# Optimization experiments

Measured on AMD Instinct MI355X. Metric: run time of the kernel, lower is better.

Reference implementation:

```python
import math
import jax, jax.numpy as jnp
import numpy as np

B, S_IN, S_OUT, D_IN, D_OUT = 8, 4096, 1024, 128, 128
EPS = 1e-5


def setup_inputs() -> dict:
    key = jax.random.key(0)
    k0, k1, k2, k3 = jax.random.split(key, 4)
    x = jax.random.normal(k0, (B, S_IN, D_IN), dtype=jnp.float32)
    M = jax.random.uniform(k1, (D_OUT, D_IN), minval=-0.5, maxval=0.5, dtype=jnp.float32)
    P = jax.random.uniform(k2, (D_OUT, D_OUT), minval=-0.1, maxval=0.1, dtype=jnp.float32)
    Linker = jax.random.uniform(k3, (S_IN, S_OUT), minval=-0.1, maxval=0.1, dtype=jnp.float32)
    gamma = jnp.ones((D_OUT,), dtype=jnp.float32)   # LayerNorm weight
    beta = jnp.zeros((D_OUT,), dtype=jnp.float32)   # LayerNorm bias
    return {"x": x, "M": M, "P": P, "Linker": Linker, "gamma": gamma, "beta": beta}


def reference(x, M, P, Linker, gamma, beta):
    # x: (B, S, in_dim) -> out: (B, S_out, out_dim)
    Bsz, S, _ = x.shape
    D = M.shape[0]
    x_trans = x @ M.T                                   # (B, S, D)
    mu = jnp.mean(x_trans, axis=-1, keepdims=True)
    var = jnp.var(x_trans, axis=-1, keepdims=True)      # biased, matches torch LayerNorm
    x_trans = (x_trans - mu) / jnp.sqrt(var + EPS) * gamma + beta
    # periods[i, j] = i*D + j + 2 (registered buffer)
    idx = jnp.arange(D)
    periods = (idx[:, None] * D + idx[None, :] + 2).astype(jnp.float32)  # (D, D)
    k = jnp.arange(S, dtype=jnp.float32)[:, None, None]                   # (S, 1, 1)
    phi = jnp.cos(2.0 * math.pi * k / periods)                            # (S, D, D)
    M_k = P[None, :, :] * phi                                             # (S, D, D)
    Nk = jnp.einsum('bsj,sij->bsi', x_trans, M_k)                         # (B, S, D)
    out = jnp.einsum('bsi,st->bti', Nk, Linker)                           # (B, S_out, D)
    return out
```

## Files before the change

### kernel.cpp

```cpp
#include <hip/hip_runtime.h>
#include <math.h>

#define B_SZ   8
#define S_INN  4096
#define S_OUTT 1024
#define DD     128
#define EPS_LN 1e-5f

typedef _Float16 h2 __attribute__((ext_vector_type(2)));
typedef _Float16 h4 __attribute__((ext_vector_type(4)));
typedef _Float16 h8 __attribute__((ext_vector_type(8)));
typedef float f32x4 __attribute__((ext_vector_type(4)));

#define XN_OFF   0
#define NK16_OFF 4194304
#define NT_OFF   6291456
#define LT_OFF   8388608

__device__ __forceinline__ void gload16(const void* g, void* l) {
    __builtin_amdgcn_global_load_lds(
        (const __attribute__((address_space(1))) unsigned int*)g,
        (__attribute__((address_space(3))) unsigned int*)l, 16, 0, 0);
}

__device__ __forceinline__ float fdot2_(h2 a, h2 b, float c) {
#if __has_builtin(__builtin_amdgcn_fdot2)
    return __builtin_amdgcn_fdot2(a, b, c, false);
#else
    return fmaf((float)a[0], (float)b[0], fmaf((float)a[1], (float)b[1], c));
#endif
}

__global__ __launch_bounds__(256) void kA(const float* __restrict__ x,
                                          const float* __restrict__ M,
                                          const float* __restrict__ gamma,
                                          const float* __restrict__ beta,
                                          _Float16* __restrict__ xn16) {
    __shared__ float Ms[128 * 128];

    const int tid = threadIdx.x;
    #pragma unroll
    for (int k = 0; k < 16; ++k) {
        int e4 = tid + k * 256;
        int i  = e4 >> 5;
        int j4 = e4 & 31;
        float4 v = *(const float4*)&M[i * DD + j4 * 4];
        int igp = (i >> 4) & 7;
        int qp  = (i >> 2) & 3;
        int cp  = i & 3;
        int col = (qp * 8 + igp) * 4 + cp;
        Ms[(j4 * 4 + 0) * 128 + col] = v.x;
        Ms[(j4 * 4 + 1) * 128 + col] = v.y;
        Ms[(j4 * 4 + 2) * 128 + col] = v.z;
        Ms[(j4 * 4 + 3) * 128 + col] = v.w;
    }
    __syncthreads();

    const int ig = tid & 7;
    const int rg = tid >> 3;
    const int row0 = blockIdx.x * 64 + rg * 2;

    float acc[2][16];
    #pragma unroll
    for (int rr = 0; rr < 2; ++rr)
        #pragma unroll
        for (int k = 0; k < 16; ++k) acc[rr][k] = 0.f;

    const float4* xr[2];
    #pragma unroll
    for (int rr = 0; rr < 2; ++rr) xr[rr] = (const float4*)&x[(size_t)(row0 + rr) * DD];

    for (int j4 = 0; j4 < 32; ++j4) {
        float xvf[2][4];
        #pragma unroll
        for (int rr = 0; rr < 2; ++rr) {
            float4 t = xr[rr][j4];
            xvf[rr][0] = t.x; xvf[rr][1] = t.y; xvf[rr][2] = t.z; xvf[rr][3] = t.w;
        }
        #pragma unroll
        for (int c = 0; c < 4; ++c) {
            const float* Mrow = &Ms[(j4 * 4 + c) * 128];
            #pragma unroll
            for (int q = 0; q < 4; ++q) {
                const float4 mv = *(const float4*)&Mrow[(q * 8 + ig) * 4];
                #pragma unroll
                for (int rr = 0; rr < 2; ++rr) {
                    acc[rr][q * 4 + 0] = fmaf(xvf[rr][c], mv.x, acc[rr][q * 4 + 0]);
                    acc[rr][q * 4 + 1] = fmaf(xvf[rr][c], mv.y, acc[rr][q * 4 + 1]);
                    acc[rr][q * 4 + 2] = fmaf(xvf[rr][c], mv.z, acc[rr][q * 4 + 2]);
                    acc[rr][q * 4 + 3] = fmaf(xvf[rr][c], mv.w, acc[rr][q * 4 + 3]);
                }
            }
        }
    }

    float g[16], be[16];
    #pragma unroll
    for (int q = 0; q < 4; ++q) {
        float4 gv = *(const float4*)&gamma[ig * 16 + q * 4];
        float4 bv = *(const float4*)&beta[ig * 16 + q * 4];
        g[q*4+0]=gv.x; g[q*4+1]=gv.y; g[q*4+2]=gv.z; g[q*4+3]=gv.w;
        be[q*4+0]=bv.x; be[q*4+1]=bv.y; be[q*4+2]=bv.z; be[q*4+3]=bv.w;
    }
    #pragma unroll
    for (int rr = 0; rr < 2; ++rr) {
        float s1 = 0.f, s2 = 0.f;
        #pragma unroll
        for (int k = 0; k < 16; ++k) { s1 += acc[rr][k]; s2 = fmaf(acc[rr][k], acc[rr][k], s2); }
        #pragma unroll
        for (int m = 1; m < 8; m <<= 1) {
            s1 += __shfl_xor(s1, m, 64);
            s2 += __shfl_xor(s2, m, 64);
        }
        float mu  = s1 * (1.f / 128.f);
        float var = s2 * (1.f / 128.f) - mu * mu;
        float rstd = rsqrtf(var + EPS_LN);
        _Float16* dst = &xn16[(size_t)(row0 + rr) * DD + ig * 16];
        #pragma unroll
        for (int q = 0; q < 4; ++q) {
            h4 hv;
            hv[0] = (_Float16)((acc[rr][q*4+0] - mu) * rstd * g[q*4+0] + be[q*4+0]);
            hv[1] = (_Float16)((acc[rr][q*4+1] - mu) * rstd * g[q*4+1] + be[q*4+1]);
            hv[2] = (_Float16)((acc[rr][q*4+2] - mu) * rstd * g[q*4+2] + be[q*4+2]);
            hv[3] = (_Float16)((acc[rr][q*4+3] - mu) * rstd * g[q*4+3] + be[q*4+3]);
            *(h4*)&dst[q * 4] = hv;
        }
    }
}

__global__ __launch_bounds__(256, 4) void kB(const _Float16* __restrict__ xn16,
                                             const float* __restrict__ P,
                                             _Float16* __restrict__ nk16) {
    const int s = blockIdx.x;
    __shared__ _Float16 Ps[128 * 136];
    __shared__ _Float16 xs[64 * 16];

    const int tid = threadIdx.x;
    {
        int j  = tid & 127;
        int bh = (tid >> 7) * 4;
        int j2 = j >> 1;
        int slot = (j2 & 15) * 4 + (j2 >> 4);
        #pragma unroll
        for (int bo = 0; bo < 4; ++bo) {
            int b = bh + bo;
            xs[slot * 16 + b * 2 + (j & 1)] = xn16[((size_t)b * S_INN + s) * DD + j];
        }
    }
    #pragma unroll
    for (int k = 0; k < 16; ++k) {
        int e4 = tid + k * 256;
        int ip = e4 >> 5, j4 = e4 & 31;
        float4 v = *(const float4*)&P[ip * DD + j4 * 4];
        h4 hv = { (_Float16)v.x, (_Float16)v.y, (_Float16)v.z, (_Float16)v.w };
        *(h4*)&Ps[ip * 136 + j4 * 4] = hv;
    }
    __syncthreads();

    const int il = tid >> 2;
    const int jq = tid & 3;
    const float kf = (float)s;
    const float pb0 = (float)(il * DD + jq * 32 + 2);

    float acc0[8] = {0.f,0.f,0.f,0.f,0.f,0.f,0.f,0.f};
    float acc1[8] = {0.f,0.f,0.f,0.f,0.f,0.f,0.f,0.f};

    #pragma unroll
    for (int j8 = 0; j8 < 4; ++j8) {
        const int j0 = jq * 32 + j8 * 8;
        h8 p0 = *(const h8*)&Ps[il * 136 + j0];
        h8 p1 = *(const h8*)&Ps[(il + 64) * 136 + j0];

        h2 w0[4], w1[4];
        #pragma unroll
        for (int cp = 0; cp < 4; ++cp) {
            float wv0[2], wv1[2];
            #pragma unroll
            for (int u = 0; u < 2; ++u) {
                int c = cp * 2 + u;
                float pf0 = pb0 + (float)(j8 * 8 + c);
                float iv0 = __builtin_amdgcn_rcpf(pf0);
                float q0  = floorf(kf * iv0);
                float rm0 = fmaf(-q0, pf0, kf);
                wv0[u] = (float)p0[c] * __builtin_amdgcn_cosf(rm0 * iv0);
                float pf1 = pf0 + 8192.f;
                float iv1 = __builtin_amdgcn_rcpf(pf1);
                float q1  = floorf(kf * iv1);
                float rm1 = fmaf(-q1, pf1, kf);
                wv1[u] = (float)p1[c] * __builtin_amdgcn_cosf(rm1 * iv1);
            }
            w0[cp] = h2{ (_Float16)wv0[0], (_Float16)wv0[1] };
            w1[cp] = h2{ (_Float16)wv1[0], (_Float16)wv1[1] };
        }

        #pragma unroll
        for (int jp = 0; jp < 4; ++jp) {
            int slot = (j8 * 4 + jp) * 4 + jq;
            const h8 xlo = *(const h8*)&xs[slot * 16];
            const h8 xhi = *(const h8*)&xs[slot * 16 + 8];
            #pragma unroll
            for (int b = 0; b < 4; ++b) {
                h2 xa = h2{ xlo[b * 2], xlo[b * 2 + 1] };
                h2 xb = h2{ xhi[b * 2], xhi[b * 2 + 1] };
                acc0[b]     = fdot2_(w0[jp], xa, acc0[b]);
                acc0[b + 4] = fdot2_(w0[jp], xb, acc0[b + 4]);
                acc1[b]     = fdot2_(w1[jp], xa, acc1[b]);
                acc1[b + 4] = fdot2_(w1[jp], xb, acc1[b + 4]);
            }
        }
    }

    #pragma unroll
    for (int m = 1; m < 4; m <<= 1) {
        #pragma unroll
        for (int b = 0; b < 8; ++b) {
            acc0[b] += __shfl_xor(acc0[b], m, 64);
            acc1[b] += __shfl_xor(acc1[b], m, 64);
        }
    }
    if (jq == 0) {
        #pragma unroll
        for (int b = 0; b < 8; ++b) {
            nk16[((size_t)b * S_INN + s) * DD + il]      = (_Float16)acc0[b];
            nk16[((size_t)b * S_INN + s) * DD + il + 64] = (_Float16)acc1[b];
        }
    }
}

__global__ __launch_bounds__(256) void kXf(const float* __restrict__ src,
                                           _Float16* __restrict__ dst,
                                           int R, int C) {
    const size_t sb = (size_t)blockIdx.z * (size_t)R * C;
    const int r0 = blockIdx.x * 64, c0 = blockIdx.y * 64;
    __shared__ float tile[64][67];
    const int tid = threadIdx.x;
    {
        const int lr = tid >> 2, lc = (tid & 3) * 16;
        const float4* srow = (const float4*)&src[sb + (size_t)(r0 + lr) * C + c0 + lc];
        float4 v0 = srow[0], v1 = srow[1], v2 = srow[2], v3 = srow[3];
        *(float4*)&tile[lr][lc +  0] = v0;
        *(float4*)&tile[lr][lc +  4] = v1;
        *(float4*)&tile[lr][lc +  8] = v2;
        *(float4*)&tile[lr][lc + 12] = v3;
    }
    __syncthreads();
    {
        const int wc = tid >> 2, wsx = (tid & 3) * 16;
        h8 o0, o1;
        #pragma unroll
        for (int k = 0; k < 8; ++k) o0[k] = (_Float16)tile[wsx + k][wc];
        #pragma unroll
        for (int k = 0; k < 8; ++k) o1[k] = (_Float16)tile[wsx + 8 + k][wc];
        _Float16* drow = &dst[sb + (size_t)(c0 + wc) * R + r0 + wsx];
        *(h8*)&drow[0] = o0;
        *(h8*)&drow[8] = o1;
    }
}

__global__ __launch_bounds__(256) void kXh(const _Float16* __restrict__ src,
                                           _Float16* __restrict__ dst,
                                           int R, int C) {
    const size_t sb = (size_t)blockIdx.z * (size_t)R * C;
    const int r0 = blockIdx.x * 64, c0 = blockIdx.y * 64;
    __shared__ _Float16 tile[64][74];
    const int tid = threadIdx.x;
    {
        const int lr = tid >> 2, lc = (tid & 3) * 16;
        const h8* srow = (const h8*)&src[sb + (size_t)(r0 + lr) * C + c0 + lc];
        h8 v0 = srow[0], v1 = srow[1];
        *(h8*)&tile[lr][lc + 0] = v0;
        *(h8*)&tile[lr][lc + 8] = v1;
    }
    __syncthreads();
    {
        const int wc = tid >> 2, wsx = (tid & 3) * 16;
        h8 o0, o1;
        #pragma unroll
        for (int k = 0; k < 8; ++k) o0[k] = tile[wsx + k][wc];
        #pragma unroll
        for (int k = 0; k < 8; ++k) o1[k] = tile[wsx + 8 + k][wc];
        _Float16* drow = &dst[sb + (size_t)(c0 + wc) * R + r0 + wsx];
        *(h8*)&drow[0] = o0;
        *(h8*)&drow[8] = o1;
    }
}

__global__ __launch_bounds__(512) void kC(const _Float16* __restrict__ NT,
                                          const _Float16* __restrict__ LT,
                                          float* __restrict__ part) {
    __shared__ _Float16 lds_pool[4 * 8192];

    const int tid  = threadIdx.x;
    const int lane = tid & 63;
    const int w    = tid >> 6;
    const int wm   = w >> 2;
    const int wn   = w & 3;
    const int lr   = lane & 15;
    const int lh   = lane >> 4;

    const int mt = blockIdx.x >> 3;
    const int nt = blockIdx.x & 7;
    const int kz = blockIdx.y;
    const int t0 = mt * 128;
    const int n0 = nt * 128;
    const int sbase = kz * 1024;

    const int swz = (lr & 7) << 4;

    f32x4 acc[4][2];
    #pragma unroll
    for (int m = 0; m < 4; ++m)
        #pragma unroll
        for (int n = 0; n < 2; ++n) acc[m][n] = (f32x4){0.f, 0.f, 0.f, 0.f};

    auto stage = [&](int buf, int s0) {
        _Float16* base = &lds_pool[buf * 16384];
        #pragma unroll
        for (int ro = 0; ro < 2; ++ro) {
            int idx = tid + ro * 512;
            int r   = idx >> 3;
            int kb  = idx & 7;
            int skb = kb ^ (r & 7);
            gload16(&LT[(size_t)(t0 + r) * S_INN + s0 + skb * 8], base + idx * 8);
            gload16(&NT[(size_t)(n0 + r) * S_INN + s0 + skb * 8], base + 8192 + idx * 8);
        }
    };

    auto compute = [&](int buf) {
        const char* ldsA = (const char*)&lds_pool[buf * 16384];
        const char* ldsB = ldsA + 16384;
        #pragma unroll
        for (int kk = 0; kk < 2; ++kk) {
            const int kb = (kk * 64 + lh * 16) ^ swz;
            h8 a[4], bf[2];
            #pragma unroll
            for (int m = 0; m < 4; ++m)
                a[m] = *(const h8*)(ldsA + (wm * 64 + m * 16 + lr) * 128 + kb);
            #pragma unroll
            for (int n = 0; n < 2; ++n)
                bf[n] = *(const h8*)(ldsB + (wn * 32 + n * 16 + lr) * 128 + kb);
            #pragma unroll
            for (int m = 0; m < 4; ++m)
                #pragma unroll
                for (int n = 0; n < 2; ++n)
                    acc[m][n] = __builtin_amdgcn_mfma_f32_16x16x32_f16(a[m], bf[n], acc[m][n], 0, 0, 0);
        }
    };

    stage(0, sbase);
    __syncthreads();
    for (int st = 0; st < 16; ++st) {
        const int cur = st & 1;
        if (st < 15) stage(cur ^ 1, sbase + (st + 1) * 64);
        compute(cur);
        __syncthreads();
    }

    float* dst = &part[(size_t)(kz * B_SZ + nt) * S_OUTT * DD];
    #pragma unroll
    for (int m = 0; m < 4; ++m) {
        const int t = t0 + wm * 64 + m * 16 + lh * 4;
        #pragma unroll
        for (int n = 0; n < 2; ++n) {
            const int i = wn * 32 + n * 16 + lr;
            #pragma unroll
            for (int r = 0; r < 4; ++r)
                dst[(size_t)(t + r) * DD + i] = acc[m][n][r];
        }
    }
}

__global__ __launch_bounds__(256) void kD(const float* __restrict__ part,
                                          float* __restrict__ out) {
    const int e4 = blockIdx.x * 256 + threadIdx.x;
    const float4* p = (const float4*)part;
    float4 a  = p[e4];
    float4 b1 = p[e4 + 262144];
    float4 c1 = p[e4 + 2 * 262144];
    float4 d1 = p[e4 + 3 * 262144];
    float4 o;
    o.x = a.x + b1.x + c1.x + d1.x;
    o.y = a.y + b1.y + c1.y + d1.y;
    o.z = a.z + b1.z + c1.z + d1.z;
    o.w = a.w + b1.w + c1.w + d1.w;
    ((float4*)out)[e4] = o;
}

extern "C" void kernel_launch(void* const* d_in, const int* in_sizes, int n_in,
                              void* d_out, int out_size, void* d_ws, size_t ws_size,
                              hipStream_t stream) {
    const float* x     = (const float*)d_in[0];
    const float* M     = (const float*)d_in[1];
    const float* P     = (const float*)d_in[2];
    const float* Lk    = (const float*)d_in[3];
    const float* gamma = (const float*)d_in[4];
    const float* beta  = (const float*)d_in[5];
    float* out = (float*)d_out;

    float* wsf = (float*)d_ws;
    _Float16*  xn16 = (_Float16*)(wsf + XN_OFF);
    _Float16*  nk16 = (_Float16*)(wsf + NK16_OFF);
    _Float16*  NT   = (_Float16*)(wsf + NT_OFF);
    _Float16*  LT   = (_Float16*)(wsf + LT_OFF);
    float*     part = wsf + XN_OFF;

    hipLaunchKernelGGL(kA,  dim3(512),        dim3(256), 0, stream, x, M, gamma, beta, xn16);
    hipLaunchKernelGGL(kB,  dim3(4096),       dim3(256), 0, stream, xn16, P, nk16);
    hipLaunchKernelGGL(kXh, dim3(64, 2, 8),   dim3(256), 0, stream, nk16, NT, S_INN, DD);
    hipLaunchKernelGGL(kXf, dim3(64, 16, 1),  dim3(256), 0, stream, Lk, LT, S_INN, S_OUTT);
    hipLaunchKernelGGL(kC,  dim3(64, 4),      dim3(512), 0, stream, NT, LT, part);
    hipLaunchKernelGGL(kD,  dim3(1024),       dim3(256), 0, stream, part, out);
}
```

Measured before the change: 176.7 us.

## Fuse Nk transpose into kB, process 8 positions per block, use fract

kB now handles eight sequence positions per block, so the P matrix is converted and staged into LDS once per eight positions rather than once per position. It writes Nk directly in the transposed (b, d, s) layout that kC consumes, which removes the separate kXh transpose kernel and its round trip through global memory. The cross-lane reduction becomes a butterfly that spreads the outputs over the four lanes instead of only lane 0, and the cos argument is built with a fract instruction in place of floor and fma. The grid shrinks to 512 blocks and the launch-bounds occupancy hint is dropped, so register pressure from the eight-position loop and lower occupancy are the risks.

```diff
diff --git a/kernel.cpp b/kernel.cpp
--- a/kernel.cpp
+++ b/kernel.cpp
@@ -13,7 +13,6 @@
 typedef float f32x4 __attribute__((ext_vector_type(4)));
 
 #define XN_OFF   0
-#define NK16_OFF 4194304
 #define NT_OFF   6291456
 #define LT_OFF   8388608
 
@@ -28,6 +27,14 @@
     return __builtin_amdgcn_fdot2(a, b, c, false);
 #else
     return fmaf((float)a[0], (float)b[0], fmaf((float)a[1], (float)b[1], c));
+#endif
+}
+
+__device__ __forceinline__ float fract_(float x) {
+#if __has_builtin(__builtin_amdgcn_fractf)
+    return __builtin_amdgcn_fractf(x);
+#else
+    return x - floorf(x);
 #endif
 }
 
@@ -128,23 +135,26 @@
     }
 }
 
-__global__ __launch_bounds__(256, 4) void kB(const _Float16* __restrict__ xn16,
-                                             const float* __restrict__ P,
-                                             _Float16* __restrict__ nk16) {
-    const int s = blockIdx.x;
+__global__ __launch_bounds__(256) void kB(const _Float16* __restrict__ xn16,
+                                          const float* __restrict__ P,
+                                          _Float16* __restrict__ NT) {
+    const int s0 = blockIdx.x * 8;
     __shared__ _Float16 Ps[128 * 136];
-    __shared__ _Float16 xs[64 * 16];
+    __shared__ _Float16 xs[8 * 1024];
 
     const int tid = threadIdx.x;
-    {
-        int j  = tid & 127;
-        int bh = (tid >> 7) * 4;
-        int j2 = j >> 1;
-        int slot = (j2 & 15) * 4 + (j2 >> 4);
-        #pragma unroll
-        for (int bo = 0; bo < 4; ++bo) {
-            int b = bh + bo;
-            xs[slot * 16 + b * 2 + (j & 1)] = xn16[((size_t)b * S_INN + s) * DD + j];
+    #pragma unroll
+    for (int k = 0; k < 4; ++k) {
+        int c   = tid + k * 256;
+        int row = c >> 4;
+        int b   = row >> 3, sl = row & 7;
+        int kk  = c & 15;
+        h8 v = *(const h8*)&xn16[((size_t)b * S_INN + s0 + sl) * DD + kk * 8];
+        #pragma unroll
+        for (int q = 0; q < 4; ++q) {
+            int j2 = kk * 4 + q;
+            int slot = (j2 & 15) * 4 + (j2 >> 4);
+            *(h2*)&xs[sl * 1024 + slot * 16 + b * 2] = h2{ v[q * 2], v[q * 2 + 1] };
         }
     }
     #pragma unroll
@@ -152,78 +162,97 @@
         int e4 = tid + k * 256;
         int ip = e4 >> 5, j4 = e4 & 31;
         float4 v = *(const float4*)&P[ip * DD + j4 * 4];
-        h4 hv = { (_Float16)v.x, (_Float16)v.y, (_Float16)v.z, (_Float16)v.w };
-        *(h4*)&Ps[ip * 136 + j4 * 4] = hv;
+        *(h4*)&Ps[ip * 136 + j4 * 4] = h4{ (_Float16)v.x, (_Float16)v.y,
+                                           (_Float16)v.z, (_Float16)v.w };
     }
     __syncthreads();
 
     const int il = tid >> 2;
     const int jq = tid & 3;
-    const float kf = (float)s;
-    const float pb0 = (float)(il * DD + jq * 32 + 2);
-
-    float acc0[8] = {0.f,0.f,0.f,0.f,0.f,0.f,0.f,0.f};
-    float acc1[8] = {0.f,0.f,0.f,0.f,0.f,0.f,0.f,0.f};
-
-    #pragma unroll
-    for (int j8 = 0; j8 < 4; ++j8) {
-        const int j0 = jq * 32 + j8 * 8;
-        h8 p0 = *(const h8*)&Ps[il * 136 + j0];
-        h8 p1 = *(const h8*)&Ps[(il + 64) * 136 + j0];
-
-        h2 w0[4], w1[4];
-        #pragma unroll
-        for (int cp = 0; cp < 4; ++cp) {
-            float wv0[2], wv1[2];
-            #pragma unroll
-            for (int u = 0; u < 2; ++u) {
-                int c = cp * 2 + u;
-                float pf0 = pb0 + (float)(j8 * 8 + c);
-                float iv0 = __builtin_amdgcn_rcpf(pf0);
-                float q0  = floorf(kf * iv0);
-                float rm0 = fmaf(-q0, pf0, kf);
-                wv0[u] = (float)p0[c] * __builtin_amdgcn_cosf(rm0 * iv0);
-                float pf1 = pf0 + 8192.f;
-                float iv1 = __builtin_amdgcn_rcpf(pf1);
-                float q1  = floorf(kf * iv1);
-                float rm1 = fmaf(-q1, pf1, kf);
-                wv1[u] = (float)p1[c] * __builtin_amdgcn_cosf(rm1 * iv1);
+    const int j0base = jq * 32;
+    const float s0f = (float)s0;
+    const float pb0 = (float)(il * DD + j0base + 2);
+    const int bsel = ((jq & 1) << 2) | (jq & 2);
+
+    h8 st[4];
+    #pragma unroll
+    for (int s_ = 0; s_ < 4; ++s_) st[s_] = h8{};
+
+    #pragma unroll
+    for (int sl = 0; sl < 8; ++sl) {
+        const float sf = s0f + (float)sl;
+        float acc0[8] = {0,0,0,0,0,0,0,0};
+        float acc1[8] = {0,0,0,0,0,0,0,0};
+
+        #pragma unroll
+        for (int j8 = 0; j8 < 4; ++j8) {
+            h8 p0 = *(const h8*)&Ps[il * 136 + j0base + j8 * 8];
+            h8 p1 = *(const h8*)&Ps[(il + 64) * 136 + j0base + j8 * 8];
+
+            h2 w0[4], w1[4];
+            #pragma unroll
+            for (int cp = 0; cp < 4; ++cp) {
+                float wv0[2], wv1[2];
+                #pragma unroll
+                for (int u = 0; u < 2; ++u) {
+                    int c = cp * 2 + u;
+                    float pf0 = pb0 + (float)(j8 * 8 + c);
+                    float r0  = fract_(sf * __builtin_amdgcn_rcpf(pf0));
+                    wv0[u] = (float)p0[c] * __builtin_amdgcn_cosf(r0);
+                    float pf1 = pf0 + 8192.f;
+                    float r1  = fract_(sf * __builtin_amdgcn_rcpf(pf1));
+                    wv1[u] = (float)p1[c] * __builtin_amdgcn_cosf(r1);
+                }
+                w0[cp] = h2{ (_Float16)wv0[0], (_Float16)wv0[1] };
+                w1[cp] = h2{ (_Float16)wv1[0], (_Float16)wv1[1] };
             }
-            w0[cp] = h2{ (_Float16)wv0[0], (_Float16)wv0[1] };
-            w1[cp] = h2{ (_Float16)wv1[0], (_Float16)wv1[1] };
-        }
-
-        #pragma unroll
-        for (int jp = 0; jp < 4; ++jp) {
-            int slot = (j8 * 4 + jp) * 4 + jq;
-            const h8 xlo = *(const h8*)&xs[slot * 16];
-            const h8 xhi = *(const h8*)&xs[slot * 16 + 8];
-            #pragma unroll
-            for (int b = 0; b < 4; ++b) {
-                h2 xa = h2{ xlo[b * 2], xlo[b * 2 + 1] };
-                h2 xb = h2{ xhi[b * 2], xhi[b * 2 + 1] };
-                acc0[b]     = fdot2_(w0[jp], xa, acc0[b]);
-                acc0[b + 4] = fdot2_(w0[jp], xb, acc0[b + 4]);
-                acc1[b]     = fdot2_(w1[jp], xa, acc1[b]);
-                acc1[b + 4] = fdot2_(w1[jp], xb, acc1[b + 4]);
+
+            #pragma unroll
+            for (int jp = 0; jp < 4; ++jp) {
+                int slot = (j8 * 4 + jp) * 4 + jq;
+                const h8 xlo = *(const h8*)&xs[sl * 1024 + slot * 16];
+                const h8 xhi = *(const h8*)&xs[sl * 1024 + slot * 16 + 8];
+                #pragma unroll
+                for (int b = 0; b < 4; ++b) {
+                    h2 xa = h2{ xlo[b * 2], xlo[b * 2 + 1] };
+                    h2 xb = h2{ xhi[b * 2], xhi[b * 2 + 1] };
+                    acc0[b]     = fdot2_(w0[jp], xa, acc0[b]);
+                    acc0[b + 4] = fdot2_(w0[jp], xb, acc0[b + 4]);
+                    acc1[b]     = fdot2_(w1[jp], xa, acc1[b]);
+                    acc1[b + 4] = fdot2_(w1[jp], xb, acc1[b + 4]);
+                }
             }
         }
-    }
-
-    #pragma unroll
-    for (int m = 1; m < 4; m <<= 1) {
-        #pragma unroll
-        for (int b = 0; b < 8; ++b) {
-            acc0[b] += __shfl_xor(acc0[b], m, 64);
-            acc1[b] += __shfl_xor(acc1[b], m, 64);
-        }
-    }
-    if (jq == 0) {
-        #pragma unroll
-        for (int b = 0; b < 8; ++b) {
-            nk16[((size_t)b * S_INN + s) * DD + il]      = (_Float16)acc0[b];
-            nk16[((size_t)b * S_INN + s) * DD + il + 64] = (_Float16)acc1[b];
-        }
+
+        const bool lo1 = (jq & 1) == 0;
+        const bool lo2 = (jq & 2) == 0;
+        float n0[4], n1[4];
+        #pragma unroll
+        for (int k = 0; k < 4; ++k) {
+            float mine   = lo1 ? acc0[k] : acc0[k + 4];
+            float theirs = lo1 ? acc0[k + 4] : acc0[k];
+            n0[k] = mine + __shfl_xor(theirs, 1, 64);
+            float mine1   = lo1 ? acc1[k] : acc1[k + 4];
+            float theirs1 = lo1 ? acc1[k + 4] : acc1[k];
+            n1[k] = mine1 + __shfl_xor(theirs1, 1, 64);
+        }
+        #pragma unroll
+        for (int k = 0; k < 2; ++k) {
+            float mine   = lo2 ? n0[k] : n0[k + 2];
+            float theirs = lo2 ? n0[k + 2] : n0[k];
+            float r0 = mine + __shfl_xor(theirs, 2, 64);
+            float mine1   = lo2 ? n1[k] : n1[k + 2];
+            float theirs1 = lo2 ? n1[k + 2] : n1[k];
+            float r1 = mine1 + __shfl_xor(theirs1, 2, 64);
+            st[k][sl]     = (_Float16)r0;
+            st[2 + k][sl] = (_Float16)r1;
+        }
+    }
+
+    #pragma unroll
+    for (int k = 0; k < 2; ++k) {
+        *(h8*)&NT[((size_t)(bsel + k) * DD + il) * S_INN + s0]        = st[k];
+        *(h8*)&NT[((size_t)(bsel + k) * DD + il + 64) * S_INN + s0]   = st[2 + k];
     }
 }
 
@@ -257,34 +286,6 @@
     }
 }
 
-__global__ __launch_bounds__(256) void kXh(const _Float16* __restrict__ src,
-                                           _Float16* __restrict__ dst,
-                                           int R, int C) {
-    const size_t sb = (size_t)blockIdx.z * (size_t)R * C;
-    const int r0 = blockIdx.x * 64, c0 = blockIdx.y * 64;
-    __shared__ _Float16 tile[64][74];
-    const int tid = threadIdx.x;
-    {
-        const int lr = tid >> 2, lc = (tid & 3) * 16;
-        const h8* srow = (const h8*)&src[sb + (size_t)(r0 + lr) * C + c0 + lc];
-        h8 v0 = srow[0], v1 = srow[1];
-        *(h8*)&tile[lr][lc + 0] = v0;
-        *(h8*)&tile[lr][lc + 8] = v1;
-    }
-    __syncthreads();
-    {
-        const int wc = tid >> 2, wsx = (tid & 3) * 16;
-        h8 o0, o1;
-        #pragma unroll
-        for (int k = 0; k < 8; ++k) o0[k] = tile[wsx + k][wc];
-        #pragma unroll
-        for (int k = 0; k < 8; ++k) o1[k] = tile[wsx + 8 + k][wc];
-        _Float16* drow = &dst[sb + (size_t)(c0 + wc) * R + r0 + wsx];
-        *(h8*)&drow[0] = o0;
-        *(h8*)&drow[8] = o1;
-    }
-}
-
 __global__ __launch_bounds__(512) void kC(const _Float16* __restrict__ NT,
                                           const _Float16* __restrict__ LT,
                                           float* __restrict__ part) {
@@ -399,14 +400,12 @@
 
     float* wsf = (float*)d_ws;
     _Float16*  xn16 = (_Float16*)(wsf + XN_OFF);
-    _Float16*  nk16 = (_Float16*)(wsf + NK16_OFF);
     _Float16*  NT   = (_Float16*)(wsf + NT_OFF);
     _Float16*  LT   = (_Float16*)(wsf + LT_OFF);
     float*     part = wsf + XN_OFF;
 
     hipLaunchKernelGGL(kA,  dim3(512),        dim3(256), 0, stream, x, M, gamma, beta, xn16);
-    hipLaunchKernelGGL(kB,  dim3(4096),       dim3(256), 0, stream, xn16, P, nk16);
-    hipLaunchKernelGGL(kXh, dim3(64, 2, 8),   dim3(256), 0, stream, nk16, NT, S_INN, DD);
+    hipLaunchKernelGGL(kB,  dim3(512),        dim3(256), 0, stream, xn16, P, NT);
     hipLaunchKernelGGL(kXf, dim3(64, 16, 1),  dim3(256), 0, stream, Lk, LT, S_INN, S_OUTT);
     hipLaunchKernelGGL(kC,  dim3(64, 4),      dim3(512), 0, stream, NT, LT, part);
     hipLaunchKernelGGL(kD,  dim3(1024),       dim3(256), 0, stream, part, out);
```

Result: faster. 169.0 us (-4.3%).
